# Performance work log

Measured on AMD Instinct MI355X. Metric: run time of the kernel, lower is better.

Reference implementation:

```python
import math
import jax, jax.numpy as jnp
import numpy as np

THETA_BINS = 8
PHI_BINS = 8
BLOCK_SIZE = 15
MAX_PHI = math.pi
DVOL = 64  # input volume is DVOL^3
EPS = 2.220446049250313e-16  # sys.float_info.epsilon


def _sobel_weight():
    # Fixed (3,1,3,3,3) central-difference kernels: channel 0 = d/dz, 1 = d/dy, 2 = d/dx
    w = np.zeros((3, 1, 3, 3, 3), np.float32)
    w[0, 0, 0, 1, 1] = -1.0; w[0, 0, 2, 1, 1] = 1.0  # s_z
    w[1, 0, 1, 0, 1] = -1.0; w[1, 0, 1, 2, 1] = 1.0  # s_y
    w[2, 0, 1, 1, 0] = -1.0; w[2, 0, 1, 1, 2] = 1.0  # s_x
    return jnp.asarray(w)


def setup_inputs() -> dict:
    key = jax.random.key(0)
    x = jax.random.normal(key, (DVOL, DVOL, DVOL), dtype=jnp.float32)
    return {"x": x, "weight": _sobel_weight()}


def reference(x, weight):
    offset = BLOCK_SIZE // 2 + 1  # 8; output spatial = d + 2*offset - 2
    xb = x.astype(jnp.float32)[None, None]  # (1,1,d,h,w)
    out = jax.lax.conv_general_dilated(
        xb, weight, window_strides=(1, 1, 1),
        padding=[(offset, offset)] * 3,
        dimension_numbers=("NCDHW", "OIDHW", "NCDHW"))[0]  # (3, D, H, W)

    mag = jnp.sqrt(jnp.sum(out * out, axis=0))              # (D,H,W) frobenius over channel
    theta = jnp.arctan2(out[1], out[2])
    phi = jnp.arccos(out[0] / (mag + EPS))

    # NOTE: original code divides theta by max_phi_angle and scales by phi_bins (faithful)
    t_raw = theta / MAX_PHI * PHI_BINS
    p_raw = phi / MAX_PHI * PHI_BINS
    t_frac = t_raw - jnp.trunc(t_raw)  # torch.frac semantics
    p_frac = p_raw - jnp.trunc(p_raw)

    i0 = jnp.floor(t_raw).astype(jnp.int32) % THETA_BINS  # theta lower bin
    i1 = jnp.ceil(t_raw).astype(jnp.int32) % THETA_BINS   # theta upper bin
    i2 = jnp.floor(p_raw).astype(jnp.int32) % PHI_BINS    # phi lower bin
    i3 = jnp.ceil(p_raw).astype(jnp.int32) % PHI_BINS     # phi upper bin

    f0 = jnp.abs(t_frac); f1 = jnp.abs(1.0 - t_frac)
    f2 = jnp.abs(p_frac); f3 = jnp.abs(1.0 - p_frac)
    w0 = (f0 * f2) * mag  # scattered to (i0, i2) via scatter_ set
    w1 = (f0 * f3) * mag  # scatter_add at (i0, i3)
    w2 = (f1 * f2) * mag  # scatter_add at (i1, i2)

    # The torch scatter_/scatter_add_ chain (zero fill elsewhere, initial tensor zeros)
    # reduces exactly to three one-hot depositions per voxel; 4th add is absent
    # because the source forward is truncated after the third scatter_add_.
    tb = jnp.arange(THETA_BINS, dtype=jnp.int32)[:, None, None, None]  # (T,1,1,1)
    pb = jnp.arange(PHI_BINS, dtype=jnp.int32)[:, None, None, None]   # (P,1,1,1)
    t0 = (tb == i0).astype(mag.dtype)  # (T,D,H,W)
    t1 = (tb == i1).astype(mag.dtype)
    p2 = (pb == i2).astype(mag.dtype)  # (P,D,H,W)
    p3 = (pb == i3).astype(mag.dtype)

    out_plus_bins = (t0[:, None] * p2[None] * w0
                     + t0[:, None] * p3[None] * w1
                     + t1[:, None] * p2[None] * w2)  # (T,P,D,H,W)
    return out_plus_bins[None]  # (1, theta_bins, phi_bins, D, H, W)
```

## Files before the change

kernel.cpp:

```cpp
#include <hip/hip_runtime.h>
#include <math.h>


#define DVOL 64
#define S 78
#define S3 (S * S * S)
#define NQ (S3 / 4)

__device__ __forceinline__ float ldx(const float* __restrict__ x, int z, int y, int xx) {
    if ((unsigned)z < (unsigned)DVOL && (unsigned)y < (unsigned)DVOL && (unsigned)xx < (unsigned)DVOL)
        return x[(z * DVOL + y) * DVOL + xx];
    return 0.0f;
}

__device__ __forceinline__ void analyze(const float* __restrict__ x, int idx,
                                        int& bo0, int& bo1, int& bo2,
                                        float& wo0, float& wo1, float& wo2) {
#pragma clang fp contract(off)
    int ox = idx % S;
    int r  = idx / S;
    int oy = r % S;
    int oz = r / S;
    int ix = ox - 7, iy = oy - 7, iz = oz - 7;

    float gz = ldx(x, iz + 1, iy, ix) - ldx(x, iz - 1, iy, ix);
    float gy = ldx(x, iz, iy + 1, ix) - ldx(x, iz, iy - 1, ix);
    float gx = ldx(x, iz, iy, ix + 1) - ldx(x, iz, iy, ix - 1);

    float mag2 = (gz * gz + gy * gy) + gx * gx;
    float mag  = sqrtf(mag2);

    bo0 = bo1 = bo2 = -1;
    wo0 = wo1 = wo2 = 0.0f;
    if (mag == 0.0f) return;

    const float EPS32 = 2.220446049250313e-16f;
    const float PI32  = 3.14159274101257324f;
    float denom = mag + EPS32;
    float ratio = gz / denom;

    float theta = atan2f(gy, gx);
    float phi   = acosf(ratio);
    float t_raw = theta / PI32 * 8.0f;
    float p_raw = phi   / PI32 * 8.0f;

    float td = fabsf(t_raw - rintf(t_raw));
    float pd = fabsf(p_raw - rintf(p_raw));
    if (td < 1e-4f || pd < 1e-4f) {
        theta = (float)atan2((double)gy, (double)gx);
        phi   = (float)acos((double)ratio);
        t_raw = theta / PI32 * 8.0f;
        p_raw = phi   / PI32 * 8.0f;
    }

    float t_frac = t_raw - truncf(t_raw);
    float p_frac = p_raw - truncf(p_raw);

    int i0 = ((int)floorf(t_raw)) & 7;
    int i1 = ((int)ceilf (t_raw)) & 7;
    int i2 = ((int)floorf(p_raw)) & 7;
    int i3 = ((int)ceilf (p_raw)) & 7;

    float f0 = fabsf(t_frac), f1 = fabsf(1.0f - t_frac);
    float f2 = fabsf(p_frac), f3 = fabsf(1.0f - p_frac);
    float w0 = (f0 * f2) * mag;
    float w1 = (f0 * f3) * mag;
    float w2 = (f1 * f2) * mag;

    int b0 = i0 * 8 + i2, b1 = i0 * 8 + i3, b2 = i1 * 8 + i2;
    if (b1 == b0) { w0 = w0 + w1; b1 = -1; }
    if (b2 == b0) { w0 = w0 + w2; b2 = -1; }

    bo0 = b0; bo1 = b1; bo2 = b2;
    wo0 = w0; wo1 = w1; wo2 = w2;
}

__global__ void __launch_bounds__(64) hog4(const float* __restrict__ x,
                                           float4* __restrict__ out4) {
    int t = blockIdx.x * 64 + threadIdx.x;
    if (t >= NQ) return;
    int base = t * 4;

    int   b[4][3];
    float w[4][3];
    #pragma unroll
    for (int v = 0; v < 4; ++v)
        analyze(x, base + v, b[v][0], b[v][1], b[v][2], w[v][0], w[v][1], w[v][2]);

    #pragma unroll
    for (int p = 0; p < 64; ++p) {
        float4 val = make_float4(0.0f, 0.0f, 0.0f, 0.0f);
        #pragma unroll
        for (int d = 0; d < 3; ++d) {
            if (b[0][d] == p) val.x = w[0][d];
            if (b[1][d] == p) val.y = w[1][d];
            if (b[2][d] == p) val.z = w[2][d];
            if (b[3][d] == p) val.w = w[3][d];
        }
        out4[(size_t)p * NQ + t] = val;
    }
}

extern "C" void kernel_launch(void* const* d_in, const int* in_sizes, int n_in,
                              void* d_out, int out_size, void* d_ws, size_t ws_size,
                              hipStream_t stream) {
    const float* x = (const float*)d_in[0];
    float4* out4 = (float4*)d_out;

    const int threads = 64;
    const int blocks = (NQ + threads - 1) / threads;
    hog4<<<blocks, threads, 0, stream>>>(x, out4);
}
```

Measured before the change: 131.3 us.

## Split HOG into per-voxel analysis pass and bin-parallel scatter pass

Splits the single fused kernel into two. The first kernel computes each voxel's gradient angles and bin weights once and stores them as a compact 8-byte record in workspace (fp16 weights plus 3-bit bin indices). The second kernel uses a 2D grid over voxel quads and the 64 bins, writing one float4 per thread. This gives much higher parallelism and coalesced stores, in exchange for an extra launch and a workspace round-trip. Storing weights in fp16 loses precision relative to the fp32 reference and may exceed tolerance.

New measurement: 132.0 us. No clear change (+0.6%).

```diff
diff --git a/kernel.cpp b/kernel.cpp
--- a/kernel.cpp
+++ b/kernel.cpp
@@ -6,6 +6,7 @@
 #define S 78
 #define S3 (S * S * S)
 #define NQ (S3 / 4)
+#define CHUNKS ((NQ + 255) / 256)
 
 __device__ __forceinline__ float ldx(const float* __restrict__ x, int z, int y, int xx) {
     if ((unsigned)z < (unsigned)DVOL && (unsigned)y < (unsigned)DVOL && (unsigned)xx < (unsigned)DVOL)
@@ -14,8 +15,8 @@
 }
 
 __device__ __forceinline__ void analyze(const float* __restrict__ x, int idx,
-                                        int& bo0, int& bo1, int& bo2,
-                                        float& wo0, float& wo1, float& wo2) {
+                                        int& i0, int& i1, int& i2, int& i3,
+                                        float& w0, float& w1, float& w2) {
 #pragma clang fp contract(off)
     int ox = idx % S;
     int r  = idx / S;
@@ -30,8 +31,8 @@
     float mag2 = (gz * gz + gy * gy) + gx * gx;
     float mag  = sqrtf(mag2);
 
-    bo0 = bo1 = bo2 = -1;
-    wo0 = wo1 = wo2 = 0.0f;
+    i0 = i1 = i2 = i3 = 0;
+    w0 = w1 = w2 = 0.0f;
     if (mag == 0.0f) return;
 
     const float EPS32 = 2.220446049250313e-16f;
@@ -56,23 +57,62 @@
     float t_frac = t_raw - truncf(t_raw);
     float p_frac = p_raw - truncf(p_raw);
 
-    int i0 = ((int)floorf(t_raw)) & 7;
-    int i1 = ((int)ceilf (t_raw)) & 7;
-    int i2 = ((int)floorf(p_raw)) & 7;
-    int i3 = ((int)ceilf (p_raw)) & 7;
+    i0 = ((int)floorf(t_raw)) & 7;
+    i1 = ((int)ceilf (t_raw)) & 7;
+    i2 = ((int)floorf(p_raw)) & 7;
+    i3 = ((int)ceilf (p_raw)) & 7;
 
     float f0 = fabsf(t_frac), f1 = fabsf(1.0f - t_frac);
     float f2 = fabsf(p_frac), f3 = fabsf(1.0f - p_frac);
-    float w0 = (f0 * f2) * mag;
-    float w1 = (f0 * f3) * mag;
-    float w2 = (f1 * f2) * mag;
+    w0 = (f0 * f2) * mag;
+    w1 = (f0 * f3) * mag;
+    w2 = (f1 * f2) * mag;
+}
 
-    int b0 = i0 * 8 + i2, b1 = i0 * 8 + i3, b2 = i1 * 8 + i2;
-    if (b1 == b0) { w0 = w0 + w1; b1 = -1; }
-    if (b2 == b0) { w0 = w0 + w2; b2 = -1; }
+__global__ void __launch_bounds__(256) hog_analyze_k(const float* __restrict__ x,
+                                                     uint2* __restrict__ rec) {
+    int idx = blockIdx.x * 256 + threadIdx.x;
+    if (idx >= S3) return;
+    int i0, i1, i2, i3; float w0, w1, w2;
+    analyze(x, idx, i0, i1, i2, i3, w0, w1, w2);
 
-    bo0 = b0; bo1 = b1; bo2 = b2;
-    wo0 = w0; wo1 = w1; wo2 = w2;
+    unsigned h0 = (unsigned)__builtin_bit_cast(unsigned short, (_Float16)w0);
+    unsigned h1 = (unsigned)__builtin_bit_cast(unsigned short, (_Float16)w1);
+    unsigned h2 = (unsigned)__builtin_bit_cast(unsigned short, (_Float16)w2);
+    uint2 rv;
+    rv.x = h0 | (h1 << 16);
+    rv.y = h2 | ((unsigned)i0 << 16) | ((unsigned)i1 << 19)
+              | ((unsigned)i2 << 22) | ((unsigned)i3 << 25);
+    rec[idx] = rv;
+}
+
+__device__ __forceinline__ float contrib(unsigned lo, unsigned hi, int p) {
+    float w0 = (float)__builtin_bit_cast(_Float16, (unsigned short)(lo & 0xffffu));
+    float w1 = (float)__builtin_bit_cast(_Float16, (unsigned short)(lo >> 16));
+    float w2 = (float)__builtin_bit_cast(_Float16, (unsigned short)(hi & 0xffffu));
+    int i0 = (hi >> 16) & 7, i1 = (hi >> 19) & 7;
+    int i2 = (hi >> 22) & 7, i3 = (hi >> 25) & 7;
+    int b0 = (i0 << 3) | i2, b1 = (i0 << 3) | i3, b2 = (i1 << 3) | i2;
+    float v = (b0 == p ? w0 : 0.0f);
+    v = v + (b1 == p ? w1 : 0.0f);
+    v = v + (b2 == p ? w2 : 0.0f);
+    return v;
+}
+
+__global__ void __launch_bounds__(256) hog_scatter_k(const uint2* __restrict__ rec,
+                                                     float4* __restrict__ out4) {
+    int q = blockIdx.x * 256 + threadIdx.x;
+    int p = blockIdx.y;
+    if (q >= NQ) return;
+    const uint4* r4 = (const uint4*)rec;
+    uint4 a = r4[q * 2];
+    uint4 b = r4[q * 2 + 1];
+    float4 val;
+    val.x = contrib(a.x, a.y, p);
+    val.y = contrib(a.z, a.w, p);
+    val.z = contrib(b.x, b.y, p);
+    val.w = contrib(b.z, b.w, p);
+    out4[(size_t)p * NQ + q] = val;
 }
 
 __global__ void __launch_bounds__(64) hog4(const float* __restrict__ x,
@@ -80,22 +120,24 @@
     int t = blockIdx.x * 64 + threadIdx.x;
     if (t >= NQ) return;
     int base = t * 4;
-
-    int   b[4][3];
-    float w[4][3];
+    int ib[4][4]; float w[4][3];
     #pragma unroll
     for (int v = 0; v < 4; ++v)
-        analyze(x, base + v, b[v][0], b[v][1], b[v][2], w[v][0], w[v][1], w[v][2]);
-
+        analyze(x, base + v, ib[v][0], ib[v][1], ib[v][2], ib[v][3],
+                w[v][0], w[v][1], w[v][2]);
     #pragma unroll
     for (int p = 0; p < 64; ++p) {
-        float4 val = make_float4(0.0f, 0.0f, 0.0f, 0.0f);
+        float4 val;
+        float* vp = (float*)&val;
         #pragma unroll
-        for (int d = 0; d < 3; ++d) {
-            if (b[0][d] == p) val.x = w[0][d];
-            if (b[1][d] == p) val.y = w[1][d];
-            if (b[2][d] == p) val.z = w[2][d];
-            if (b[3][d] == p) val.w = w[3][d];
+        for (int v = 0; v < 4; ++v) {
+            int b0 = (ib[v][0] << 3) | ib[v][2];
+            int b1 = (ib[v][0] << 3) | ib[v][3];
+            int b2 = (ib[v][1] << 3) | ib[v][2];
+            float s = (b0 == p ? w[v][0] : 0.0f);
+            s = s + (b1 == p ? w[v][1] : 0.0f);
+            s = s + (b2 == p ? w[v][2] : 0.0f);
+            vp[v] = s;
         }
         out4[(size_t)p * NQ + t] = val;
     }
@@ -107,7 +149,11 @@
     const float* x = (const float*)d_in[0];
     float4* out4 = (float4*)d_out;
 
-    const int threads = 64;
-    const int blocks = (NQ + threads - 1) / threads;
-    hog4<<<blocks, threads, 0, stream>>>(x, out4);
+    if (ws_size >= (size_t)S3 * 8) {
+        uint2* rec = (uint2*)d_ws;
+        hog_analyze_k<<<(S3 + 255) / 256, 256, 0, stream>>>(x, rec);
+        hog_scatter_k<<<dim3(CHUNKS, 64), 256, 0, stream>>>(rec, out4);
+    } else {
+        hog4<<<(NQ + 63) / 64, 64, 0, stream>>>(x, out4);
+    }
 }
```

## Split bin output across a second grid dimension and use nontemporal stores

Applied to the files above, without the earlier changes.

The kernel now launches a 2D grid in which each block handles 8 of the 64 output bins for 4 voxels per thread, using 256-thread blocks, so there are 8x more threads each writing fewer planes. Every thread recomputes the gradient, the angles and the bin indices for its 4 voxels, which means that analysis is done 8 times per voxel. Output writes go through nontemporal vector stores to avoid polluting the cache with the large write-only output. The per-voxel merge of duplicate bins is replaced by summing the three conditional contributions per bin.

New measurement: 145.9 us. 11.1% more time.

```diff
diff --git a/kernel.cpp b/kernel.cpp
--- a/kernel.cpp
+++ b/kernel.cpp
@@ -7,6 +7,8 @@
 #define S3 (S * S * S)
 #define NQ (S3 / 4)
 
+typedef float f32x4 __attribute__((ext_vector_type(4)));
+
 __device__ __forceinline__ float ldx(const float* __restrict__ x, int z, int y, int xx) {
     if ((unsigned)z < (unsigned)DVOL && (unsigned)y < (unsigned)DVOL && (unsigned)xx < (unsigned)DVOL)
         return x[(z * DVOL + y) * DVOL + xx];
@@ -14,8 +16,8 @@
 }
 
 __device__ __forceinline__ void analyze(const float* __restrict__ x, int idx,
-                                        int& bo0, int& bo1, int& bo2,
-                                        float& wo0, float& wo1, float& wo2) {
+                                        int& i0, int& i1, int& i2, int& i3,
+                                        float& w0, float& w1, float& w2) {
 #pragma clang fp contract(off)
     int ox = idx % S;
     int r  = idx / S;
@@ -30,8 +32,8 @@
     float mag2 = (gz * gz + gy * gy) + gx * gx;
     float mag  = sqrtf(mag2);
 
-    bo0 = bo1 = bo2 = -1;
-    wo0 = wo1 = wo2 = 0.0f;
+    i0 = i1 = i2 = i3 = 0;
+    w0 = w1 = w2 = 0.0f;
     if (mag == 0.0f) return;
 
     const float EPS32 = 2.220446049250313e-16f;
@@ -56,48 +58,48 @@
     float t_frac = t_raw - truncf(t_raw);
     float p_frac = p_raw - truncf(p_raw);
 
-    int i0 = ((int)floorf(t_raw)) & 7;
-    int i1 = ((int)ceilf (t_raw)) & 7;
-    int i2 = ((int)floorf(p_raw)) & 7;
-    int i3 = ((int)ceilf (p_raw)) & 7;
+    i0 = ((int)floorf(t_raw)) & 7;
+    i1 = ((int)ceilf (t_raw)) & 7;
+    i2 = ((int)floorf(p_raw)) & 7;
+    i3 = ((int)ceilf (p_raw)) & 7;
 
     float f0 = fabsf(t_frac), f1 = fabsf(1.0f - t_frac);
     float f2 = fabsf(p_frac), f3 = fabsf(1.0f - p_frac);
-    float w0 = (f0 * f2) * mag;
-    float w1 = (f0 * f3) * mag;
-    float w2 = (f1 * f2) * mag;
-
-    int b0 = i0 * 8 + i2, b1 = i0 * 8 + i3, b2 = i1 * 8 + i2;
-    if (b1 == b0) { w0 = w0 + w1; b1 = -1; }
-    if (b2 == b0) { w0 = w0 + w2; b2 = -1; }
-
-    bo0 = b0; bo1 = b1; bo2 = b2;
-    wo0 = w0; wo1 = w1; wo2 = w2;
+    w0 = (f0 * f2) * mag;
+    w1 = (f0 * f3) * mag;
+    w2 = (f1 * f2) * mag;
 }
 
-__global__ void __launch_bounds__(64) hog4(const float* __restrict__ x,
-                                           float4* __restrict__ out4) {
-    int t = blockIdx.x * 64 + threadIdx.x;
-    if (t >= NQ) return;
-    int base = t * 4;
+__global__ void __launch_bounds__(256) hog8(const float* __restrict__ x,
+                                            f32x4* __restrict__ out4) {
+    int q = blockIdx.x * 256 + threadIdx.x;
+    if (q >= NQ) return;
+    int pg = blockIdx.y * 8;
+    int base = q * 4;
 
-    int   b[4][3];
-    float w[4][3];
+    int bb[4][3]; float ww[4][3];
     #pragma unroll
-    for (int v = 0; v < 4; ++v)
-        analyze(x, base + v, b[v][0], b[v][1], b[v][2], w[v][0], w[v][1], w[v][2]);
+    for (int v = 0; v < 4; ++v) {
+        int i0, i1, i2, i3; float w0, w1, w2;
+        analyze(x, base + v, i0, i1, i2, i3, w0, w1, w2);
+        bb[v][0] = (i0 << 3) | i2;
+        bb[v][1] = (i0 << 3) | i3;
+        bb[v][2] = (i1 << 3) | i2;
+        ww[v][0] = w0; ww[v][1] = w1; ww[v][2] = w2;
+    }
 
     #pragma unroll
-    for (int p = 0; p < 64; ++p) {
-        float4 val = make_float4(0.0f, 0.0f, 0.0f, 0.0f);
+    for (int d = 0; d < 8; ++d) {
+        int p = pg + d;
+        f32x4 val;
         #pragma unroll
-        for (int d = 0; d < 3; ++d) {
-            if (b[0][d] == p) val.x = w[0][d];
-            if (b[1][d] == p) val.y = w[1][d];
-            if (b[2][d] == p) val.z = w[2][d];
-            if (b[3][d] == p) val.w = w[3][d];
+        for (int v = 0; v < 4; ++v) {
+            float s = (bb[v][0] == p ? ww[v][0] : 0.0f);
+            s = s + (bb[v][1] == p ? ww[v][1] : 0.0f);
+            s = s + (bb[v][2] == p ? ww[v][2] : 0.0f);
+            val[v] = s;
         }
-        out4[(size_t)p * NQ + t] = val;
+        __builtin_nontemporal_store(val, &out4[(size_t)p * NQ + q]);
     }
 }
 
@@ -105,9 +107,7 @@
                               void* d_out, int out_size, void* d_ws, size_t ws_size,
                               hipStream_t stream) {
     const float* x = (const float*)d_in[0];
-    float4* out4 = (float4*)d_out;
+    f32x4* out4 = (f32x4*)d_out;
 
-    const int threads = 64;
-    const int blocks = (NQ + threads - 1) / threads;
-    hog4<<<blocks, threads, 0, stream>>>(x, out4);
+    hog8<<<dim3((NQ + 255) / 256, 8), 256, 0, stream>>>(x, out4);
 }
```
